# Kernel optimization log

Hardware: AMD Instinct MI355X
Metric: run time of the kernel (lower is better)

The kernel has to match this reference:

```python
import jax, jax.numpy as jnp
import numpy as np

B_SZ, N_NODES, C_IN, C_OUT, M_EDGES, DEG = 32, 4096, 64, 64, 64, 256
E_INC = M_EDGES * DEG  # 16384 incidences
NEG_SLOPE = 0.2
MARGIN = 4.2


def setup_inputs() -> dict:
    key = jax.random.key(0)
    k1, k2, k3, k4 = jax.random.split(key, 4)
    x = jax.random.normal(k1, (B_SZ, N_NODES, C_IN), jnp.float32)
    # glorot-ish params
    weight = jax.random.normal(k2, (C_IN, C_OUT), jnp.float32) * (1.0 / np.sqrt(C_IN))
    att = jax.random.normal(k3, (1, 1, 2 * C_OUT), jnp.float32) * 0.1
    node_ids = jax.random.randint(k4, (E_INC,), 0, N_NODES, dtype=jnp.int32)
    edge_ids = jnp.repeat(jnp.arange(M_EDGES, dtype=jnp.int32), DEG)  # sorted, all edges present
    hyperedge_index = jnp.stack([node_ids, edge_ids], axis=0)
    return {"x": x, "weight": weight, "att": att,
            "hyperedge_index": hyperedge_index,
            "num_edges": M_EDGES, "num_nodes": N_NODES}


def _segment_softmax(scores, seg, num_segments):
    m = jax.ops.segment_max(scores, seg, num_segments=num_segments)
    e = jnp.exp(scores - m[seg])
    s = jax.ops.segment_sum(e, seg, num_segments=num_segments)
    return e / s[seg]


def reference(x, weight, att, hyperedge_index, num_edges, num_nodes):
    node_ids = hyperedge_index[0]
    edge_ids = hyperedge_index[1]
    M = num_edges
    N = num_nodes

    xw = jnp.einsum('bnc,cd->bnd', x, weight)       # [B,N,C]
    x1 = jnp.swapaxes(xw, 0, 1)                     # [N,B,C]

    x_i = x1[node_ids]                              # [E,B,C] gather per incidence
    edge_sums = jax.ops.segment_sum(x_i, edge_ids, num_segments=M,
                                    indices_are_sorted=True)  # [M,B,C]
    x_j = edge_sums[edge_ids]                       # [E,B,C]

    # pairwise hyperedge contrastive loss (vectorized double loop over edges)
    inner = jnp.einsum('kbc,mbc->kmb', edge_sums, edge_sums)          # [M,M,B]
    nrm = jnp.linalg.norm(edge_sums, axis=-1)                         # [M,B]
    cos = inner / (nrm[:, None, :] * nrm[None, :, :])                 # [M,M,B]
    diff = edge_sums[:, None] - edge_sums[None, :]                    # [M,M,B,C]
    dist = jnp.linalg.norm(diff, axis=-1)                             # [M,M,B]
    loss_item = cos * dist + (1.0 - cos) * jnp.clip(MARGIN - dist, 0.0)
    loss_hyper = jnp.sum(jnp.abs(jnp.mean(loss_item, axis=2))) / (M + 1) ** 2

    # GAT-style attention over incidences, softmax grouped by node
    cat = jnp.concatenate([x_i, x_j], axis=-1)                        # [E,B,2C]
    scores = jnp.sum(cat * att[0], axis=-1)                           # [E,B] (heads=1)
    scores = jax.nn.leaky_relu(scores, negative_slope=NEG_SLOPE)
    alpha = _segment_softmax(scores, node_ids, N)                     # [E,B]
    # dropout omitted (eval mode)

    ones = jnp.ones((node_ids.shape[0],), xw.dtype)
    D = jax.ops.segment_sum(ones, node_ids, num_segments=N)           # node degree
    deg_e = jax.ops.segment_sum(ones, edge_ids, num_segments=M, indices_are_sorted=True)
    B_norm = jnp.where(deg_e > 0, 1.0 / deg_e, 0.0)                   # 1/edge degree, inf->0

    # stage 1: nodes -> hyperedges (source_to_target)
    msg1 = B_norm[edge_ids][:, None, None] * (alpha[..., None] * x_i) # [E,B,C]
    out_e = jax.ops.segment_sum(msg1, edge_ids, num_segments=M, indices_are_sorted=True)
    # stage 2: hyperedges -> nodes (target_to_source)
    msg2 = D[node_ids][:, None, None] * (alpha[..., None] * out_e[edge_ids])
    out_n = jax.ops.segment_sum(msg2, node_ids, num_segments=N)       # [N,B,C]

    out = jnp.swapaxes(out_n, 0, 1)                                   # [B,N,C]
    constrain_total = jnp.abs(jnp.mean(x_i - x_j)) + loss_hyper
    return out, constrain_total
```

## Files before the change

kernel.cpp:

```cpp
#include <hip/hip_runtime.h>
#include <hip/hip_fp16.h>
#include <math.h>

#define B_SZ 32
#define N_NODES 4096
#define C_DIM 64
#define M_EDGES 64
#define DEG 256
#define E_INC 16384
#define NEG_SLOPE 0.2f
#define MARGIN 4.2f

__device__ __forceinline__ float wsum64(float v) {
#pragma unroll
  for (int off = 32; off > 0; off >>= 1) v += __shfl_xor(v, off, 64);
  return v;
}

__global__ __launch_bounds__(256) void k_p0(
    const float* __restrict__ x, const float* __restrict__ w,
    const float* __restrict__ att, const int* __restrict__ node_ids,
    float* __restrict__ s1_t, __half* __restrict__ xh,
    int* __restrict__ cntv) {
  const int bid = blockIdx.x;
  const int t = threadIdx.x;
  if (bid < 512) {
    __shared__ float part[4][64];
    __shared__ float wattl[64];
    const int kk = t & 63, q = t >> 6;
    float p = 0.f;
#pragma unroll
    for (int c = 0; c < 16; ++c)
      p = fmaf(w[kk * 64 + q * 16 + c], att[q * 16 + c], p);
    part[q][kk] = p;
    __syncthreads();
    if (t < 64)
      wattl[t] = part[0][t] + part[1][t] + part[2][t] + part[3][t];
    __syncthreads();
    const int lane = t & 63, wv = t >> 6;
    const int kq = lane & 15, rsub = lane >> 4;
    const float4 wq = ((const float4*)wattl)[kq];
    const int r0 = bid * 256 + wv * 64;
#pragma unroll 4
    for (int it = 0; it < 16; ++it) {
      const int row = r0 + it * 4 + rsub;
      const float4 xv = ((const float4*)x)[row * 16 + kq];
      float vv = xv.x * wq.x + xv.y * wq.y + xv.z * wq.z + xv.w * wq.w;
      vv += __shfl_xor(vv, 1, 64);
      vv += __shfl_xor(vv, 2, 64);
      vv += __shfl_xor(vv, 4, 64);
      vv += __shfl_xor(vv, 8, 64);
      if (kq == 0) {
        const int n = row & (N_NODES - 1);
        const int b = row >> 12;
        s1_t[n * 32 + b] = vv;
      }
      union {
        __half2 h2[2];
        uint2 u;
      } pk;
      pk.h2[0] = __halves2half2(__float2half(xv.x), __float2half(xv.y));
      pk.h2[1] = __halves2half2(__float2half(xv.z), __float2half(xv.w));
      ((uint2*)xh)[row * 16 + kq] = pk.u;
    }
  } else {
    __shared__ int cnt[N_NODES];
    const int m = bid - 512;
#pragma unroll
    for (int i = 0; i < 16; ++i) cnt[t + 256 * i] = 0;
    __syncthreads();
    atomicAdd(&cnt[node_ids[m * DEG + t]], 1);
    __syncthreads();
#pragma unroll
    for (int i = 0; i < 16; ++i)
      cntv[m * N_NODES + t + 256 * i] = cnt[t + 256 * i];
  }
}

__global__ __launch_bounds__(256) void k_p1(
    const __half* __restrict__ xh, const float* __restrict__ w,
    const float* __restrict__ att, const int* __restrict__ node_ids,
    float* __restrict__ es_t, float* __restrict__ s2,
    float* __restrict__ nrm2, float* __restrict__ essum) {
  __shared__ float wl[4096];
  __shared__ float sx[4][4][64];
  __shared__ float est[4][64];
  const int bid = blockIdx.x;
  const int bg = bid & 7;
  const int m = bid >> 3;
  const int b0 = bg * 4;
  const int t = threadIdx.x;
  const int lane = t & 63, wv = t >> 6;
  const int co = lane & 7, rg = lane >> 3;
  float4* wl4 = (float4*)wl;
  const float4* w4 = (const float4*)w;
#pragma unroll
  for (int i = 0; i < 4; ++i) wl4[t + 256 * i] = w4[t + 256 * i];
  const int myinc = node_ids[m * DEG + wv * 64 + lane];
  int nds[8];
#pragma unroll
  for (int j = 0; j < 8; ++j) nds[j] = __shfl(myinc, j * 8 + rg, 64);
#pragma unroll
  for (int bi = 0; bi < 4; ++bi) {
    const uint4* xb =
        (const uint4*)(xh + (size_t)(b0 + bi) * (N_NODES * C_DIM));
    uint4 v[8];
#pragma unroll
    for (int j = 0; j < 8; ++j) v[j] = xb[nds[j] * 8 + co];
    float acc[8] = {0.f, 0.f, 0.f, 0.f, 0.f, 0.f, 0.f, 0.f};
#pragma unroll
    for (int j = 0; j < 8; ++j) {
      const __half2* hp = (const __half2*)&v[j];
#pragma unroll
      for (int q = 0; q < 4; ++q) {
        const float2 f2 = __half22float2(hp[q]);
        acc[2 * q] += f2.x;
        acc[2 * q + 1] += f2.y;
      }
    }
#pragma unroll
    for (int off = 8; off < 64; off <<= 1) {
#pragma unroll
      for (int k = 0; k < 8; ++k) acc[k] += __shfl_xor(acc[k], off, 64);
    }
    if (rg == 0) {
      ((float4*)&sx[wv][bi][co * 8])[0] =
          make_float4(acc[0], acc[1], acc[2], acc[3]);
      ((float4*)&sx[wv][bi][co * 8])[1] =
          make_float4(acc[4], acc[5], acc[6], acc[7]);
    }
  }
  __syncthreads();
  {
    const int c = lane;
    float es = 0.f;
#pragma unroll 8
    for (int j = 0; j < 64; ++j) {
      const float sxcj =
          sx[0][wv][j] + sx[1][wv][j] + sx[2][wv][j] + sx[3][wv][j];
      es = fmaf(sxcj, wl[j * 64 + c], es);
    }
    est[wv][c] = es;
    const float sr = wsum64(es * att[64 + c]);
    const float nr = wsum64(es * es);
    const float er = wsum64(es);
    if (c == 0) {
      s2[m * 32 + b0 + wv] = sr;
      nrm2[m * 32 + b0 + wv] = nr;
      essum[m * 32 + b0 + wv] = er;
    }
  }
  __syncthreads();
  if (t < 64) {
    const float4 o = make_float4(est[0][t], est[1][t], est[2][t], est[3][t]);
    *(float4*)&es_t[(m * 64 + t) * 32 + b0] = o;
  }
}

__global__ __launch_bounds__(256) void k_p2(
    const float* __restrict__ es_t, const float* __restrict__ nrm2,
    const int* __restrict__ cntv, const float* __restrict__ s1_t,
    const float* __restrict__ s2, float* __restrict__ lossbuf2,
    float2* __restrict__ pnb, int* __restrict__ pdat,
    int* __restrict__ plen) {
  const int bid = blockIdx.x;
  if (bid < 504) {
    const int wv = threadIdx.x >> 6;
    const int p = bid * 4 + wv;
    int k = 0, off = 0;
    while (off + (63 - k) <= p) {
      off += 63 - k;
      ++k;
    }
    const int m = k + 1 + (p - off);
    const int lane = threadIdx.x & 63;
    const int b = lane & 31, ch = lane >> 5;
    float inner = 0.f;
#pragma unroll 8
    for (int cc = 0; cc < 32; ++cc) {
      const int c = cc + 32 * ch;
      inner = fmaf(es_t[(k * 64 + c) * 32 + b], es_t[(m * 64 + c) * 32 + b],
                   inner);
    }
    inner += __shfl_xor(inner, 32, 64);
    const float nk2 = nrm2[k * 32 + b];
    const float nm2 = nrm2[m * 32 + b];
    const float d2 = fmaxf(nk2 + nm2 - 2.f * inner, 0.f);
    const float dist = sqrtf(d2);
    const float cosv = inner / sqrtf(nk2 * nm2);
    float li = cosv * dist + (1.f - cosv) * fmaxf(MARGIN - dist, 0.f);
#pragma unroll
    for (int o = 16; o > 0; o >>= 1) li += __shfl_xor(li, o, 64);
    if (lane == 0) lossbuf2[p] = 2.f * fabsf(li * (1.f / 32.f));
  } else {
    const int idx = (bid - 504) * 256 + threadIdx.x;
    const int n = idx >> 5, b = idx & 31;
    const float s1v = s1_t[n * 32 + b];
    const bool leader = (b == 0);
    float mx = -1e30f, S = 0.f;
    int j = 0, Dsum = 0;
#pragma unroll 4
    for (int m = 0; m < 64; ++m) {
      const int cm = cntv[m * N_NODES + n];
      float sc = s1v + s2[m * 32 + b];
      sc = sc > 0.f ? sc : NEG_SLOPE * sc;
      const float scv = (cm > 0) ? sc : -1e30f;
      const float nm = fmaxf(mx, scv);
      S = S * __expf(mx - nm) + (float)cm * __expf(scv - nm);
      mx = nm;
      if (leader) {
        if (cm > 0) {
          pdat[n * 64 + j] = m | (cm << 8);
          ++j;
        }
        Dsum += cm;
      }
    }
    if (leader) plen[n] = j | (Dsum << 7);
    float2 pv;
    pv.x = mx;
    pv.y = (S > 0.f) ? 1.f / S : 0.f;
    pnb[n * 32 + b] = pv;
  }
}

__global__ __launch_bounds__(256) void k_p3(
    const __half* __restrict__ xh, const int* __restrict__ node_ids,
    const float* __restrict__ w, const float* __restrict__ s1_t,
    const float* __restrict__ s2, const float2* __restrict__ pnb,
    const float* __restrict__ essum, const float* __restrict__ lossbuf2,
    float* __restrict__ out_e_t, float* __restrict__ outs) {
  __shared__ float wl[4096];
  __shared__ float sx[4][4][64];
  __shared__ float est[4][64];
  const int bid = blockIdx.x;
  const int t = threadIdx.x;
  if (bid < 512) {
    const int bg = bid & 7;
    const int m = bid >> 3;
    const int b0 = bg * 4;
    const int lane = t & 63, wv = t >> 6;
    const int co = lane & 7, rg = lane >> 3;
    float4* wl4 = (float4*)wl;
    const float4* w4 = (const float4*)w;
#pragma unroll
    for (int i = 0; i < 4; ++i) wl4[t + 256 * i] = w4[t + 256 * i];
    const int myinc = node_ids[m * DEG + wv * 64 + lane];
    const float4 s14 = *(const float4*)&s1_t[myinc * 32 + b0];
    const float* pp = (const float*)&pnb[myinc * 32 + b0];
    const float4 pA = *(const float4*)pp;
    const float4 pB = *(const float4*)(pp + 4);
    float mya[4];
    {
      const float s1a[4] = {s14.x, s14.y, s14.z, s14.w};
      const float mxa[4] = {pA.x, pA.z, pB.x, pB.z};
      const float iva[4] = {pA.y, pA.w, pB.y, pB.w};
#pragma unroll
      for (int bi = 0; bi < 4; ++bi) {
        float sc = s1a[bi] + s2[m * 32 + b0 + bi];
        sc = sc > 0.f ? sc : NEG_SLOPE * sc;
        mya[bi] = __expf(sc - mxa[bi]) * iva[bi];
      }
    }
    int nds[8];
#pragma unroll
    for (int j = 0; j < 8; ++j) nds[j] = __shfl(myinc, j * 8 + rg, 64);
#pragma unroll
    for (int bi = 0; bi < 4; ++bi) {
      const uint4* xb =
          (const uint4*)(xh + (size_t)(b0 + bi) * (N_NODES * C_DIM));
      float av[8];
#pragma unroll
      for (int j = 0; j < 8; ++j) av[j] = __shfl(mya[bi], j * 8 + rg, 64);
      uint4 v[8];
#pragma unroll
      for (int j = 0; j < 8; ++j) v[j] = xb[nds[j] * 8 + co];
      float acc[8] = {0.f, 0.f, 0.f, 0.f, 0.f, 0.f, 0.f, 0.f};
#pragma unroll
      for (int j = 0; j < 8; ++j) {
        const __half2* hp = (const __half2*)&v[j];
#pragma unroll
        for (int q = 0; q < 4; ++q) {
          const float2 f2 = __half22float2(hp[q]);
          acc[2 * q] = fmaf(av[j], f2.x, acc[2 * q]);
          acc[2 * q + 1] = fmaf(av[j], f2.y, acc[2 * q + 1]);
        }
      }
#pragma unroll
      for (int off = 8; off < 64; off <<= 1) {
#pragma unroll
        for (int k = 0; k < 8; ++k) acc[k] += __shfl_xor(acc[k], off, 64);
      }
      if (rg == 0) {
        ((float4*)&sx[wv][bi][co * 8])[0] =
            make_float4(acc[0], acc[1], acc[2], acc[3]);
        ((float4*)&sx[wv][bi][co * 8])[1] =
            make_float4(acc[4], acc[5], acc[6], acc[7]);
      }
    }
    __syncthreads();
    {
      const int c = lane;
      float oc = 0.f;
#pragma unroll 8
      for (int j = 0; j < 64; ++j) {
        const float sxcj =
            sx[0][wv][j] + sx[1][wv][j] + sx[2][wv][j] + sx[3][wv][j];
        oc = fmaf(sxcj, wl[j * 64 + c], oc);
      }
      est[wv][c] = oc * (1.0f / 256.0f);
    }
    __syncthreads();
    if (t < 64) {
      const float4 o =
          make_float4(est[0][t], est[1][t], est[2][t], est[3][t]);
      *(float4*)&out_e_t[(m * 64 + t) * 32 + b0] = o;
    }
  } else {
    __shared__ float smf[256];
    float s = 0.f;
    for (int i = t; i < M_EDGES * B_SZ; i += 256) s += essum[i];
    smf[t] = s;
    __syncthreads();
    for (int o = 128; o > 0; o >>= 1) {
      if (t < o) smf[t] += smf[t + o];
      __syncthreads();
    }
    const float S = smf[0];
    __syncthreads();
    float l = 0.f;
    for (int i = t; i < 2016; i += 256) l += lossbuf2[i];
    smf[t] = l;
    __syncthreads();
    for (int o = 128; o > 0; o >>= 1) {
      if (t < o) smf[t] += smf[t + o];
      __syncthreads();
    }
    if (t == 0) {
      const float mean = S * (-255.0f) / 33554432.0f;
      outs[0] = fabsf(mean) + smf[0] * (1.0f / 4225.0f);
    }
  }
}

__global__ __launch_bounds__(256) void k_p4(
    const int* __restrict__ plen, const int* __restrict__ pdat,
    const float* __restrict__ s1_t, const float* __restrict__ s2,
    const float2* __restrict__ pnb, const float* __restrict__ out_e_t,
    float* __restrict__ out) {
  __shared__ int lme[64];
  __shared__ float lcnt[64];
  __shared__ float al[64][32];
  const int n = blockIdx.x;
  const int t = threadIdx.x;
  const int pl = plen[n];
  const int len = pl & 127;
  const float Dn = (float)(pl >> 7);
  const int c = t & 63, bq = t >> 6;
  const size_t nb = (size_t)n * 64 + c;
  const size_t st = (size_t)N_NODES * 64;
  if (len == 0) {
#pragma unroll
    for (int j = 0; j < 8; ++j) out[(bq * 8 + j) * st + nb] = 0.f;
    return;
  }
  if (t < len) {
    const int pe = pdat[n * 64 + t];
    lme[t] = pe & 63;
    lcnt[t] = (float)(pe >> 8);
  }
  __syncthreads();
  {
    const int b = t & 31, lq = t >> 5;
    const float s1v = s1_t[n * 32 + b];
    const float2 pv = pnb[n * 32 + b];
    for (int base = 0; base < len; base += 8) {
      const int li = base + lq;
      if (li < len) {
        const int m = lme[li];
        float sc = s1v + s2[m * 32 + b];
        sc = sc > 0.f ? sc : NEG_SLOPE * sc;
        al[li][b] = lcnt[li] * __expf(sc - pv.x) * pv.y;
      }
    }
  }
  __syncthreads();
  float4 a0 = {0.f, 0.f, 0.f, 0.f}, a1 = {0.f, 0.f, 0.f, 0.f};
  for (int li = 0; li < len; ++li) {
    const int m = lme[li];
    const float4 v0 = *(const float4*)&out_e_t[(m * 64 + c) * 32 + bq * 8];
    const float4 v1 = *(const float4*)&out_e_t[(m * 64 + c) * 32 + bq * 8 + 4];
    const float* alr = al[li];
    a0.x = fmaf(alr[bq * 8 + 0], v0.x, a0.x);
    a0.y = fmaf(alr[bq * 8 + 1], v0.y, a0.y);
    a0.z = fmaf(alr[bq * 8 + 2], v0.z, a0.z);
    a0.w = fmaf(alr[bq * 8 + 3], v0.w, a0.w);
    a1.x = fmaf(alr[bq * 8 + 4], v1.x, a1.x);
    a1.y = fmaf(alr[bq * 8 + 5], v1.y, a1.y);
    a1.z = fmaf(alr[bq * 8 + 6], v1.z, a1.z);
    a1.w = fmaf(alr[bq * 8 + 7], v1.w, a1.w);
  }
  out[(bq * 8 + 0) * st + nb] = Dn * a0.x;
  out[(bq * 8 + 1) * st + nb] = Dn * a0.y;
  out[(bq * 8 + 2) * st + nb] = Dn * a0.z;
  out[(bq * 8 + 3) * st + nb] = Dn * a0.w;
  out[(bq * 8 + 4) * st + nb] = Dn * a1.x;
  out[(bq * 8 + 5) * st + nb] = Dn * a1.y;
  out[(bq * 8 + 6) * st + nb] = Dn * a1.z;
  out[(bq * 8 + 7) * st + nb] = Dn * a1.w;
}

extern "C" void kernel_launch(void* const* d_in, const int* in_sizes, int n_in,
                              void* d_out, int out_size, void* d_ws,
                              size_t ws_size, hipStream_t stream) {
  (void)in_sizes; (void)n_in; (void)out_size; (void)ws_size;
  const float* x = (const float*)d_in[0];
  const float* weight = (const float*)d_in[1];
  const float* att = (const float*)d_in[2];
  const int* node_ids = (const int*)d_in[3];
  float* out = (float*)d_out;

  char* wsb = (char*)d_ws;
  float* es_t = (float*)(wsb);
  float* out_e_t = (float*)(wsb + (512 << 10));
  float* s1_t = (float*)(wsb + (1024 << 10));
  int* cntv = (int*)(wsb + (1536 << 10));
  float2* pnb = (float2*)(wsb + (2560 << 10));
  int* pdat = (int*)(wsb + (3584 << 10));
  float* s2 = (float*)(wsb + (4608 << 10));
  float* nrm2 = (float*)(wsb + (4616 << 10));
  float* essum = (float*)(wsb + (4624 << 10));
  float* lossbuf2 = (float*)(wsb + (4632 << 10));
  int* plen = (int*)(wsb + (4640 << 10));
  __half* xh = (__half*)(wsb + (5120 << 10));

  k_p0<<<576, 256, 0, stream>>>(x, weight, att, node_ids, s1_t, xh, cntv);
  k_p1<<<512, 256, 0, stream>>>(xh, weight, att, node_ids, es_t, s2, nrm2,
                                essum);
  k_p2<<<1016, 256, 0, stream>>>(es_t, nrm2, cntv, s1_t, s2, lossbuf2, pnb,
                                 pdat, plen);
  k_p3<<<513, 256, 0, stream>>>(xh, node_ids, weight, s1_t, s2, pnb, essum,
                                lossbuf2, out_e_t,
                                out + (size_t)B_SZ * N_NODES * C_DIM);
  k_p4<<<4096, 256, 0, stream>>>(plen, pdat, s1_t, s2, pnb, out_e_t, out);
}
```

Baseline: 84.45 us.

## Drop fp16 staging copy of x and fuse edge-sum gather into first kernel

The fp16 copy of x, made in the first kernel and read by the edge-sum and aggregation kernels, is removed. Both gathers now read fp32 x directly with float4 loads. The edge-sum computation (old k_p1) is merged as extra blocks into the first kernel, which removes one launch and the write/read of the half buffer. In exchange each gather moves twice the bytes per row, and the merged kernel's blocks now have unequal workloads.

Measured after the change: 81.09 us, median of 2. 4.0% less time.

```diff
diff --git a/kernel.cpp b/kernel.cpp
--- a/kernel.cpp
+++ b/kernel.cpp
@@ -1,5 +1,4 @@
 #include <hip/hip_runtime.h>
-#include <hip/hip_fp16.h>
 #include <math.h>
 
 #define B_SZ 32
@@ -17,13 +16,34 @@
   return v;
 }
 
-__global__ __launch_bounds__(256) void k_p0(
+__device__ __forceinline__ float4 redq16_32(float4 a) {
+#pragma unroll
+  for (int off = 16; off < 64; off <<= 1) {
+    a.x += __shfl_xor(a.x, off, 64);
+    a.y += __shfl_xor(a.y, off, 64);
+    a.z += __shfl_xor(a.z, off, 64);
+    a.w += __shfl_xor(a.w, off, 64);
+  }
+  return a;
+}
+
+union U16K {
+  float wl[4096];
+  int cnt[4096];
+};
+
+__global__ __launch_bounds__(256) void k_pA(
     const float* __restrict__ x, const float* __restrict__ w,
     const float* __restrict__ att, const int* __restrict__ node_ids,
-    float* __restrict__ s1_t, __half* __restrict__ xh,
-    int* __restrict__ cntv) {
+    float* __restrict__ s1_t, float* __restrict__ es_t,
+    float* __restrict__ s2, float* __restrict__ nrm2,
+    float* __restrict__ essum, int* __restrict__ cntv) {
+  __shared__ U16K u;
+  __shared__ float sx[4][4][64];
+  __shared__ float est[4][64];
   const int bid = blockIdx.x;
   const int t = threadIdx.x;
+  const int lane = t & 63, wv = t >> 6;
   if (bid < 512) {
     __shared__ float part[4][64];
     __shared__ float wattl[64];
@@ -37,7 +57,6 @@
     if (t < 64)
       wattl[t] = part[0][t] + part[1][t] + part[2][t] + part[3][t];
     __syncthreads();
-    const int lane = t & 63, wv = t >> 6;
     const int kq = lane & 15, rsub = lane >> 4;
     const float4 wq = ((const float4*)wattl)[kq];
     const int r0 = bid * 256 + wv * 64;
@@ -55,109 +74,80 @@
         const int b = row >> 12;
         s1_t[n * 32 + b] = vv;
       }
-      union {
-        __half2 h2[2];
-        uint2 u;
-      } pk;
-      pk.h2[0] = __halves2half2(__float2half(xv.x), __float2half(xv.y));
-      pk.h2[1] = __halves2half2(__float2half(xv.z), __float2half(xv.w));
-      ((uint2*)xh)[row * 16 + kq] = pk.u;
-    }
+    }
+  } else if (bid < 576) {
+    const int m = bid - 512;
+#pragma unroll
+    for (int i = 0; i < 16; ++i) u.cnt[t + 256 * i] = 0;
+    __syncthreads();
+    atomicAdd(&u.cnt[node_ids[m * DEG + t]], 1);
+    __syncthreads();
+#pragma unroll
+    for (int i = 0; i < 16; ++i)
+      cntv[m * N_NODES + t + 256 * i] = u.cnt[t + 256 * i];
   } else {
-    __shared__ int cnt[N_NODES];
-    const int m = bid - 512;
-#pragma unroll
-    for (int i = 0; i < 16; ++i) cnt[t + 256 * i] = 0;
-    __syncthreads();
-    atomicAdd(&cnt[node_ids[m * DEG + t]], 1);
-    __syncthreads();
-#pragma unroll
-    for (int i = 0; i < 16; ++i)
-      cntv[m * N_NODES + t + 256 * i] = cnt[t + 256 * i];
-  }
-}
-
-__global__ __launch_bounds__(256) void k_p1(
-    const __half* __restrict__ xh, const float* __restrict__ w,
-    const float* __restrict__ att, const int* __restrict__ node_ids,
-    float* __restrict__ es_t, float* __restrict__ s2,
-    float* __restrict__ nrm2, float* __restrict__ essum) {
-  __shared__ float wl[4096];
-  __shared__ float sx[4][4][64];
-  __shared__ float est[4][64];
-  const int bid = blockIdx.x;
-  const int bg = bid & 7;
-  const int m = bid >> 3;
-  const int b0 = bg * 4;
-  const int t = threadIdx.x;
-  const int lane = t & 63, wv = t >> 6;
-  const int co = lane & 7, rg = lane >> 3;
-  float4* wl4 = (float4*)wl;
-  const float4* w4 = (const float4*)w;
-#pragma unroll
-  for (int i = 0; i < 4; ++i) wl4[t + 256 * i] = w4[t + 256 * i];
-  const int myinc = node_ids[m * DEG + wv * 64 + lane];
-  int nds[8];
-#pragma unroll
-  for (int j = 0; j < 8; ++j) nds[j] = __shfl(myinc, j * 8 + rg, 64);
-#pragma unroll
-  for (int bi = 0; bi < 4; ++bi) {
-    const uint4* xb =
-        (const uint4*)(xh + (size_t)(b0 + bi) * (N_NODES * C_DIM));
-    uint4 v[8];
-#pragma unroll
-    for (int j = 0; j < 8; ++j) v[j] = xb[nds[j] * 8 + co];
-    float acc[8] = {0.f, 0.f, 0.f, 0.f, 0.f, 0.f, 0.f, 0.f};
-#pragma unroll
-    for (int j = 0; j < 8; ++j) {
-      const __half2* hp = (const __half2*)&v[j];
-#pragma unroll
-      for (int q = 0; q < 4; ++q) {
-        const float2 f2 = __half22float2(hp[q]);
-        acc[2 * q] += f2.x;
-        acc[2 * q + 1] += f2.y;
-      }
-    }
-#pragma unroll
-    for (int off = 8; off < 64; off <<= 1) {
-#pragma unroll
-      for (int k = 0; k < 8; ++k) acc[k] += __shfl_xor(acc[k], off, 64);
-    }
-    if (rg == 0) {
-      ((float4*)&sx[wv][bi][co * 8])[0] =
-          make_float4(acc[0], acc[1], acc[2], acc[3]);
-      ((float4*)&sx[wv][bi][co * 8])[1] =
-          make_float4(acc[4], acc[5], acc[6], acc[7]);
-    }
-  }
-  __syncthreads();
-  {
-    const int c = lane;
-    float es = 0.f;
+    const int eb = bid - 576;
+    const int b0 = (eb & 7) * 4;
+    const int m = eb >> 3;
+    const int qc = lane & 15, rg = lane >> 4;
+    float4* wl4 = (float4*)u.wl;
+    const float4* w4 = (const float4*)w;
+#pragma unroll
+    for (int i = 0; i < 4; ++i) wl4[t + 256 * i] = w4[t + 256 * i];
+    const int myinc = node_ids[m * DEG + wv * 64 + lane];
+    int nds[16];
+#pragma unroll
+    for (int i = 0; i < 16; ++i) nds[i] = __shfl(myinc, i * 4 + rg, 64);
+#pragma unroll
+    for (int bi = 0; bi < 4; ++bi) {
+      const float4* xb4 =
+          (const float4*)(x + (size_t)(b0 + bi) * (N_NODES * C_DIM));
+      float4 acc = {0.f, 0.f, 0.f, 0.f};
+#pragma unroll
+      for (int h = 0; h < 2; ++h) {
+        float4 v[8];
+#pragma unroll
+        for (int j = 0; j < 8; ++j) v[j] = xb4[nds[h * 8 + j] * 16 + qc];
+#pragma unroll
+        for (int j = 0; j < 8; ++j) {
+          acc.x += v[j].x;
+          acc.y += v[j].y;
+          acc.z += v[j].z;
+          acc.w += v[j].w;
+        }
+      }
+      acc = redq16_32(acc);
+      if (rg == 0) ((float4*)&sx[wv][bi][0])[qc] = acc;
+    }
+    __syncthreads();
+    {
+      const int c = lane;
+      float es = 0.f;
 #pragma unroll 8
-    for (int j = 0; j < 64; ++j) {
-      const float sxcj =
-          sx[0][wv][j] + sx[1][wv][j] + sx[2][wv][j] + sx[3][wv][j];
-      es = fmaf(sxcj, wl[j * 64 + c], es);
-    }
-    est[wv][c] = es;
-    const float sr = wsum64(es * att[64 + c]);
-    const float nr = wsum64(es * es);
-    const float er = wsum64(es);
-    if (c == 0) {
-      s2[m * 32 + b0 + wv] = sr;
-      nrm2[m * 32 + b0 + wv] = nr;
-      essum[m * 32 + b0 + wv] = er;
-    }
-  }
-  __syncthreads();
-  if (t < 64) {
-    const float4 o = make_float4(est[0][t], est[1][t], est[2][t], est[3][t]);
-    *(float4*)&es_t[(m * 64 + t) * 32 + b0] = o;
-  }
-}
-
-__global__ __launch_bounds__(256) void k_p2(
+      for (int j = 0; j < 64; ++j) {
+        const float sxcj =
+            sx[0][wv][j] + sx[1][wv][j] + sx[2][wv][j] + sx[3][wv][j];
+        es = fmaf(sxcj, u.wl[j * 64 + c], es);
+      }
+      est[wv][c] = es;
+      const float sr = wsum64(es * att[64 + c]);
+      const float nr = wsum64(es * es);
+      const float er = wsum64(es);
+      if (c == 0) {
+        s2[m * 32 + b0 + wv] = sr;
+        nrm2[m * 32 + b0 + wv] = nr;
+        essum[m * 32 + b0 + wv] = er;
+      }
+    }
+    __syncthreads();
+    if (t < 64) {
+      const float4 o = make_float4(est[0][t], est[1][t], est[2][t], est[3][t]);
+      *(float4*)&es_t[(m * 64 + t) * 32 + b0] = o;
+    }
+  }
+}
+
+__global__ __launch_bounds__(256) void k_pB(
     const float* __restrict__ es_t, const float* __restrict__ nrm2,
     const int* __restrict__ cntv, const float* __restrict__ s1_t,
     const float* __restrict__ s2, float* __restrict__ lossbuf2,
@@ -224,8 +214,8 @@
   }
 }
 
-__global__ __launch_bounds__(256) void k_p3(
-    const __half* __restrict__ xh, const int* __restrict__ node_ids,
+__global__ __launch_bounds__(256) void k_pC(
+    const float* __restrict__ x, const int* __restrict__ node_ids,
     const float* __restrict__ w, const float* __restrict__ s1_t,
     const float* __restrict__ s2, const float2* __restrict__ pnb,
     const float* __restrict__ essum, const float* __restrict__ lossbuf2,
@@ -236,11 +226,10 @@
   const int bid = blockIdx.x;
   const int t = threadIdx.x;
   if (bid < 512) {
-    const int bg = bid & 7;
+    const int b0 = (bid & 7) * 4;
     const int m = bid >> 3;
-    const int b0 = bg * 4;
     const int lane = t & 63, wv = t >> 6;
-    const int co = lane & 7, rg = lane >> 3;
+    const int qc = lane & 15, rg = lane >> 4;
     float4* wl4 = (float4*)wl;
     const float4* w4 = (const float4*)w;
 #pragma unroll
@@ -262,58 +251,50 @@
         mya[bi] = __expf(sc - mxa[bi]) * iva[bi];
       }
     }
-    int nds[8];
-#pragma unroll
-    for (int j = 0; j < 8; ++j) nds[j] = __shfl(myinc, j * 8 + rg, 64);
+    int nds[16];
+#pragma unroll
+    for (int i = 0; i < 16; ++i) nds[i] = __shfl(myinc, i * 4 + rg, 64);
 #pragma unroll
     for (int bi = 0; bi < 4; ++bi) {
-      const uint4* xb =
-          (const uint4*)(xh + (size_t)(b0 + bi) * (N_NODES * C_DIM));
-      float av[8];
-#pragma unroll
-      for (int j = 0; j < 8; ++j) av[j] = __shfl(mya[bi], j * 8 + rg, 64);
-      uint4 v[8];
-#pragma unroll
-      for (int j = 0; j < 8; ++j) v[j] = xb[nds[j] * 8 + co];
-      float acc[8] = {0.f, 0.f, 0.f, 0.f, 0.f, 0.f, 0.f, 0.f};
-#pragma unroll
-      for (int j = 0; j < 8; ++j) {
-        const __half2* hp = (const __half2*)&v[j];
-#pragma unroll
-        for (int q = 0; q < 4; ++q) {
-          const float2 f2 = __half22float2(hp[q]);
-          acc[2 * q] = fmaf(av[j], f2.x, acc[2 * q]);
-          acc[2 * q + 1] = fmaf(av[j], f2.y, acc[2 * q + 1]);
+      const float4* xb4 =
+          (const float4*)(x + (size_t)(b0 + bi) * (N_NODES * C_DIM));
+      float4 acc = {0.f, 0.f, 0.f, 0.f};
+#pragma unroll
+      for (int h = 0; h < 2; ++h) {
+        float4 v[8];
+        float av[8];
+#pragma unroll
+        for (int j = 0; j < 8; ++j) {
+          av[j] = __shfl(mya[bi], (h * 8 + j) * 4 + rg, 64);
+          v[j] = xb4[nds[h * 8 + j] * 16 + qc];
         }
-      }
-#pragma unroll
-      for (int off = 8; off < 64; off <<= 1) {
-#pragma unroll
-        for (int k = 0; k < 8; ++k) acc[k] += __shfl_xor(acc[k], off, 64);
-      }
-      if (rg == 0) {
-        ((float4*)&sx[wv][bi][co * 8])[0] =
-            make_float4(acc[0], acc[1], acc[2], acc[3]);
-        ((float4*)&sx[wv][bi][co * 8])[1] =
-            make_float4(acc[4], acc[5], acc[6], acc[7]);
-      }
+#pragma unroll
+        for (int j = 0; j < 8; ++j) {
+          acc.x = fmaf(av[j], v[j].x, acc.x);
+          acc.y = fmaf(av[j], v[j].y, acc.y);
+          acc.z = fmaf(av[j], v[j].z, acc.z);
+          acc.w = fmaf(av[j], v[j].w, acc.w);
+        }
+      }
+      acc = redq16_32(acc);
+      if (rg == 0) ((float4*)&sx[wv][bi][0])[qc] = acc;
     }
     __syncthreads();
     {
-      const int c = lane;
+      const int c = t & 63;
+      const int wv2 = t >> 6;
       float oc = 0.f;
 #pragma unroll 8
       for (int j = 0; j < 64; ++j) {
         const float sxcj =
-            sx[0][wv][j] + sx[1][wv][j] + sx[2][wv][j] + sx[3][wv][j];
+            sx[0][wv2][j] + sx[1][wv2][j] + sx[2][wv2][j] + sx[3][wv2][j];
         oc = fmaf(sxcj, wl[j * 64 + c], oc);
       }
-      est[wv][c] = oc * (1.0f / 256.0f);
+      est[wv2][c] = oc * (1.0f / 256.0f);
     }
     __syncthreads();
     if (t < 64) {
-      const float4 o =
-          make_float4(est[0][t], est[1][t], est[2][t], est[3][t]);
+      const float4 o = make_float4(est[0][t], est[1][t], est[2][t], est[3][t]);
       *(float4*)&out_e_t[(m * 64 + t) * 32 + b0] = o;
     }
   } else {
@@ -343,7 +324,7 @@
   }
 }
 
-__global__ __launch_bounds__(256) void k_p4(
+__global__ __launch_bounds__(256) void k_pD(
     const int* __restrict__ plen, const int* __restrict__ pdat,
     const float* __restrict__ s1_t, const float* __restrict__ s2,
     const float2* __restrict__ pnb, const float* __restrict__ out_e_t,
@@ -432,15 +413,13 @@
   float* essum = (float*)(wsb + (4624 << 10));
   float* lossbuf2 = (float*)(wsb + (4632 << 10));
   int* plen = (int*)(wsb + (4640 << 10));
-  __half* xh = (__half*)(wsb + (5120 << 10));
-
-  k_p0<<<576, 256, 0, stream>>>(x, weight, att, node_ids, s1_t, xh, cntv);
-  k_p1<<<512, 256, 0, stream>>>(xh, weight, att, node_ids, es_t, s2, nrm2,
-                                essum);
-  k_p2<<<1016, 256, 0, stream>>>(es_t, nrm2, cntv, s1_t, s2, lossbuf2, pnb,
+
+  k_pA<<<1088, 256, 0, stream>>>(x, weight, att, node_ids, s1_t, es_t, s2,
+                                 nrm2, essum, cntv);
+  k_pB<<<1016, 256, 0, stream>>>(es_t, nrm2, cntv, s1_t, s2, lossbuf2, pnb,
                                  pdat, plen);
-  k_p3<<<513, 256, 0, stream>>>(xh, node_ids, weight, s1_t, s2, pnb, essum,
+  k_pC<<<513, 256, 0, stream>>>(x, node_ids, weight, s1_t, s2, pnb, essum,
                                 lossbuf2, out_e_t,
                                 out + (size_t)B_SZ * N_NODES * C_DIM);
-  k_p4<<<4096, 256, 0, stream>>>(plen, pdat, s1_t, s2, pnb, out_e_t, out);
-}
+  k_pD<<<4096, 256, 0, stream>>>(plen, pdat, s1_t, s2, pnb, out_e_t, out);
+}
```
